# Kernel optimization log

Hardware: AMD Instinct MI355X
Metric: run time of the kernel (lower is better)

Reference implementation:

```python
import jax, jax.numpy as jnp
import numpy as np

B, T, C, HS = 4, 2048, 1024, 64

def setup_inputs() -> dict:
    key = jax.random.key(0)
    k1, k2, k3, k4 = jax.random.split(key, 4)
    x = jax.random.normal(k1, (B, T, C), dtype=jnp.float32)
    # torch Linear default init scale ~ 1/sqrt(fan_in); scale weights similarly
    s = C ** -0.5
    Wq = jax.random.normal(k2, (C, HS), dtype=jnp.float32) * s
    Wk = jax.random.normal(k3, (C, HS), dtype=jnp.float32) * s
    Wv = jax.random.normal(k4, (C, HS), dtype=jnp.float32) * s
    return {"x": x, "Wq": Wq, "Wk": Wk, "Wv": Wv}

def reference(x, Wq, Wk, Wv):
    B_, T_, C_ = x.shape
    q = x @ Wq          # [B,T,HS]
    k = x @ Wk          # [B,T,HS]
    v = x @ Wv          # [B,T,HS]
    scale = C_ ** -0.5  # note: module scales by input dim C, not head_size
    w = jnp.einsum('bqh,bkh->bqk', q, k) * scale  # [B,T,T]
    causal = jnp.tril(jnp.ones((T_, T_), dtype=bool))
    w = jnp.where(causal, w, -jnp.inf)
    a = jax.nn.softmax(w, axis=-1)  # dropout is identity (eval / drop_rate=0)
    return jnp.einsum('bqk,bkh->bqh', a, v)
```

## Files before the change

### kernel.cpp

```cpp
#include <hip/hip_runtime.h>
#include <math.h>

#define B_  4
#define T_  2048
#define C_  1024
#define HS_ 64
#define M_  (B_*T_)
#define NCAT 192
#define SCALE_ 0.03125f

typedef unsigned short ushort_t;
typedef short bf16x8 __attribute__((ext_vector_type(8)));
typedef float f32x4 __attribute__((ext_vector_type(4)));

static __device__ __forceinline__ unsigned short f2bf(float f) {
    union { float f; unsigned int u; } c; c.f = f;
    unsigned int u = c.u;
    return (unsigned short)((u + 0x7FFFu + ((u >> 16) & 1u)) >> 16);
}
static __device__ __forceinline__ unsigned short f2bf_fast(float f) {
    union { float f; unsigned int u; } c; c.f = f;
    return (unsigned short)((c.u + 0x8000u) >> 16);
}

__global__ void wconv_kernel(const float* __restrict__ Wq, const float* __restrict__ Wk,
                             const float* __restrict__ Wv, ushort_t* __restrict__ wt) {
    int idx = (blockIdx.x * 256 + threadIdx.x) * 4;
    int n = idx >> 10;
    int k0 = idx & 1023;
    const float* W = (n < 64) ? Wq : (n < 128) ? Wk : Wv;
    int nn = n & 63;
    ushort_t o0 = f2bf(W[(k0 + 0) * HS_ + nn]);
    ushort_t o1 = f2bf(W[(k0 + 1) * HS_ + nn]);
    ushort_t o2 = f2bf(W[(k0 + 2) * HS_ + nn]);
    ushort_t o3 = f2bf(W[(k0 + 3) * HS_ + nn]);
    uint2 d;
    d.x = (unsigned)o0 | ((unsigned)o1 << 16);
    d.y = (unsigned)o2 | ((unsigned)o3 << 16);
    *(uint2*)(wt + (size_t)n * C_ + k0) = d;
}

__global__ __launch_bounds__(512, 4) void proj_kernel(const float* __restrict__ x,
    const ushort_t* __restrict__ wt,
    ushort_t* __restrict__ qws, ushort_t* __restrict__ kws, ushort_t* __restrict__ vt) {
    __shared__ __align__(16) f32x4 red[4][12 * 64];

    int tid  = threadIdx.x;
    int wid  = tid >> 6;
    int lane = tid & 63;
    int qd   = lane >> 4;
    int lq   = lane & 15;
    int r0   = blockIdx.x * 16;

    f32x4 acc[12];
    #pragma unroll
    for (int i = 0; i < 12; i++) acc[i] = (f32x4){0.f,0.f,0.f,0.f};

    const float*    xp = x  + (size_t)(r0 + lq) * C_ + wid * 128 + qd * 8;
    const ushort_t* wp = wt + (size_t)lq * C_ + wid * 128 + qd * 8;

    #pragma unroll
    for (int i = 0; i < 4; i++) {
        float4 a0 = *(const float4*)(xp + i * 32);
        float4 a1 = *(const float4*)(xp + i * 32 + 4);
        union { bf16x8 v; ushort_t u[8]; } af;
        af.u[0] = f2bf(a0.x); af.u[1] = f2bf(a0.y); af.u[2] = f2bf(a0.z); af.u[3] = f2bf(a0.w);
        af.u[4] = f2bf(a1.x); af.u[5] = f2bf(a1.y); af.u[6] = f2bf(a1.z); af.u[7] = f2bf(a1.w);
        #pragma unroll
        for (int nt = 0; nt < 12; nt++) {
            bf16x8 bv = *(const bf16x8*)(wp + (size_t)nt * 16 * C_ + i * 32);
            acc[nt] = __builtin_amdgcn_mfma_f32_16x16x32_bf16(af.v, bv, acc[nt], 0, 0, 0);
        }
    }

    if (wid >= 4) {
        #pragma unroll
        for (int nt = 0; nt < 12; nt++) red[wid - 4][nt * 64 + lane] = acc[nt];
    }
    __syncthreads();
    if (wid < 4) {
        #pragma unroll
        for (int nt = 0; nt < 12; nt++) acc[nt] += red[wid][nt * 64 + lane];
    }
    __syncthreads();
    if (wid == 2 || wid == 3) {
        #pragma unroll
        for (int nt = 0; nt < 12; nt++) red[wid][nt * 64 + lane] = acc[nt];
    }
    __syncthreads();
    if (wid < 2) {
        #pragma unroll
        for (int nt = 0; nt < 12; nt++) acc[nt] += red[wid + 2][nt * 64 + lane];
    }
    __syncthreads();
    if (wid == 1) {
        #pragma unroll
        for (int nt = 0; nt < 12; nt++) red[0][nt * 64 + lane] = acc[nt];
    }
    __syncthreads();
    if (wid == 0) {
        #pragma unroll
        for (int nt = 0; nt < 12; nt++) {
            acc[nt] += red[0][nt * 64 + lane];
            int outn = nt >> 2;
            int col  = (nt & 3) * 16 + lq;
            #pragma unroll
            for (int r = 0; r < 4; r++) {
                int row = r0 + qd * 4 + r;
                float v = acc[nt][r];
                if (outn == 0) v *= SCALE_;
                ushort_t val = f2bf(v);
                if (outn == 0)      qws[(size_t)row * HS_ + col] = val;
                else if (outn == 1) kws[(size_t)row * HS_ + col] = val;
                else {
                    int b = row >> 11, t = row & 2047;
                    vt[((size_t)b * 64 + col) * T_ + t] = val;
                }
            }
        }
    }
}

__global__ __launch_bounds__(1024) void flash_kernel(const ushort_t* __restrict__ qws,
    const ushort_t* __restrict__ kws, const ushort_t* __restrict__ vt,
    float* __restrict__ out) {
    __shared__ __align__(16) unsigned char pool[36864];

    int tid  = threadIdx.x;
    int wid  = tid >> 6;
    int lane = tid & 63;
    int qd   = lane >> 4;
    int lq   = lane & 15;
    int ts   = wid >> 3;
    int ws   = wid & 7;

    int batch = blockIdx.y;
    int p     = blockIdx.x;
    int tile  = ts ? (127 - p) : p;
    int q0    = tile * 16;
    int qrow  = q0 + lq;
    int grow  = batch * T_ + qrow;
    int nU    = (q0 + 16 + 63) >> 6;

    bf16x8 qf[2];
    #pragma unroll
    for (int st = 0; st < 2; st++)
        qf[st] = *(const bf16x8*)(qws + (size_t)grow * HS_ + st * 32 + qd * 8);

    float lsum = 0.f;
    f32x4 O[4];
    #pragma unroll
    for (int nt = 0; nt < 4; nt++) O[nt] = (f32x4){0.f,0.f,0.f,0.f};

    ushort_t* pw = (ushort_t*)pool + wid * 1152 + lq * 72;
    const ushort_t* kp    = kws + (size_t)batch * T_ * HS_;
    const ushort_t* vbase = vt  + (size_t)batch * 64 * T_;

    for (int u = ws; u < nU; u += 8) {
        int kb = u * 64;

        bf16x8 kf[8];
        #pragma unroll
        for (int sub = 0; sub < 4; sub++)
            #pragma unroll
            for (int st = 0; st < 2; st++)
                kf[sub * 2 + st] = *(const bf16x8*)(kp + (size_t)(kb + sub * 16 + lq) * HS_ + st * 32 + qd * 8);

        f32x4 S[4];
        #pragma unroll
        for (int sub = 0; sub < 4; sub++) {
            f32x4 s = (f32x4){0.f,0.f,0.f,0.f};
            #pragma unroll
            for (int st = 0; st < 2; st++)
                s = __builtin_amdgcn_mfma_f32_16x16x32_bf16(kf[sub * 2 + st], qf[st], s, 0, 0, 0);
            S[sub] = s;
        }

        bf16x8 vf[8];
        #pragma unroll
        for (int nt = 0; nt < 4; nt++)
            #pragma unroll
            for (int kk = 0; kk < 2; kk++)
                vf[nt * 2 + kk] = *(const bf16x8*)(vbase + ((size_t)nt * 16 + lq) * T_ + kb + kk * 32 + qd * 8);

        if (kb + 64 > q0) {
            #pragma unroll
            for (int sub = 0; sub < 4; sub++)
                #pragma unroll
                for (int r = 0; r < 4; r++) {
                    int key = kb + sub * 16 + qd * 4 + r;
                    float pv = (key <= qrow) ? __expf(S[sub][r]) : 0.f;
                    S[sub][r] = pv;
                    lsum += pv;
                }
        } else {
            #pragma unroll
            for (int sub = 0; sub < 4; sub++)
                #pragma unroll
                for (int r = 0; r < 4; r++) {
                    float pv = __expf(S[sub][r]);
                    S[sub][r] = pv;
                    lsum += pv;
                }
        }

        #pragma unroll
        for (int sub = 0; sub < 4; sub++) {
            uint2 d;
            d.x = (unsigned)f2bf_fast(S[sub][0]) | ((unsigned)f2bf_fast(S[sub][1]) << 16);
            d.y = (unsigned)f2bf_fast(S[sub][2]) | ((unsigned)f2bf_fast(S[sub][3]) << 16);
            *(uint2*)(pw + sub * 16 + qd * 4) = d;
        }
        bf16x8 pf0 = *(const bf16x8*)(pw + qd * 8);
        bf16x8 pf1 = *(const bf16x8*)(pw + 32 + qd * 8);

        #pragma unroll
        for (int nt = 0; nt < 4; nt++) {
            O[nt] = __builtin_amdgcn_mfma_f32_16x16x32_bf16(vf[nt * 2 + 0], pf0, O[nt], 0, 0, 0);
            O[nt] = __builtin_amdgcn_mfma_f32_16x16x32_bf16(vf[nt * 2 + 1], pf1, O[nt], 0, 0, 0);
        }
    }

    f32x4* red  = (f32x4*)pool;
    float* lred = (float*)(pool + 32768);
    __syncthreads();
    if (ws >= 4) {
        int sl = ts * 4 + (ws - 4);
        f32x4* rs = red + (size_t)sl * 256;
        #pragma unroll
        for (int nt = 0; nt < 4; nt++) rs[nt * 64 + lane] = O[nt];
        lred[sl * 64 + lane] = lsum;
    }
    __syncthreads();
    if (ws < 4) {
        int sl = ts * 4 + ws;
        f32x4* rs = red + (size_t)sl * 256;
        #pragma unroll
        for (int nt = 0; nt < 4; nt++) O[nt] += rs[nt * 64 + lane];
        lsum += lred[sl * 64 + lane];
    }
    __syncthreads();
    if (ws == 2 || ws == 3) {
        int sl = ts * 4 + (ws - 2);
        f32x4* rs = red + (size_t)sl * 256;
        #pragma unroll
        for (int nt = 0; nt < 4; nt++) rs[nt * 64 + lane] = O[nt];
        lred[sl * 64 + lane] = lsum;
    }
    __syncthreads();
    if (ws < 2) {
        int sl = ts * 4 + ws;
        f32x4* rs = red + (size_t)sl * 256;
        #pragma unroll
        for (int nt = 0; nt < 4; nt++) O[nt] += rs[nt * 64 + lane];
        lsum += lred[sl * 64 + lane];
    }
    __syncthreads();
    if (ws == 1) {
        int sl = ts * 4;
        f32x4* rs = red + (size_t)sl * 256;
        #pragma unroll
        for (int nt = 0; nt < 4; nt++) rs[nt * 64 + lane] = O[nt];
        lred[sl * 64 + lane] = lsum;
    }
    __syncthreads();
    if (ws == 0) {
        int sl = ts * 4;
        f32x4* rs = red + (size_t)sl * 256;
        #pragma unroll
        for (int nt = 0; nt < 4; nt++) O[nt] += rs[nt * 64 + lane];
        lsum += lred[sl * 64 + lane];
        lsum += __shfl_xor(lsum, 16, 64);
        lsum += __shfl_xor(lsum, 32, 64);
        float li = 1.f / lsum;
        #pragma unroll
        for (int nt = 0; nt < 4; nt++) {
            f32x4 o = O[nt] * li;
            *(f32x4*)(out + (size_t)grow * HS_ + nt * 16 + qd * 4) = o;
        }
    }
}

extern "C" void kernel_launch(void* const* d_in, const int* in_sizes, int n_in,
                              void* d_out, int out_size, void* d_ws, size_t ws_size,
                              hipStream_t stream) {
    const float* x  = (const float*)d_in[0];
    const float* Wq = (const float*)d_in[1];
    const float* Wk = (const float*)d_in[2];
    const float* Wv = (const float*)d_in[3];
    float* out = (float*)d_out;

    ushort_t* wt  = (ushort_t*)d_ws;
    ushort_t* qws = wt  + (size_t)NCAT * C_;
    ushort_t* kws = qws + (size_t)M_ * HS_;
    ushort_t* vt  = kws + (size_t)M_ * HS_;

    wconv_kernel<<<NCAT * C_ / (256 * 4), 256, 0, stream>>>(Wq, Wk, Wv, wt);
    proj_kernel<<<512, 512, 0, stream>>>(x, wt, qws, kws, vt);
    flash_kernel<<<dim3(64, 4), 1024, 0, stream>>>(qws, kws, vt, out);
}
```

Before: 122.2 us.

## Fuse projection and flash attention into one kernel with per-tile ready flags

Merges the QKV projection kernel and the flash-attention kernel into a single 512-block launch. Each block first projects 16 rows and publishes a release flag, then runs attention for one 16-row query tile, spinning until the K/V tiles it needs are flagged ready. Work is spread by pairing tiles from the two halves of the sequence across blocks, with 8 waves per block instead of 16. V fragment loads are also split into two halves with a scheduling barrier to cut register pressure. The cost being targeted is the kernel boundary and the tail idle time between projection and attention; the risk is spin-wait deadlock or stalls if dependent blocks are not yet resident, and fewer waves per attention tile.

After: 383.2 us. 3.14x slower.

```diff
diff --git a/kernel.cpp b/kernel.cpp
--- a/kernel.cpp
+++ b/kernel.cpp
@@ -24,7 +24,12 @@
 }
 
 __global__ void wconv_kernel(const float* __restrict__ Wq, const float* __restrict__ Wk,
-                             const float* __restrict__ Wv, ushort_t* __restrict__ wt) {
+                             const float* __restrict__ Wv, ushort_t* __restrict__ wt,
+                             int* __restrict__ flags) {
+    if (blockIdx.x == 0) {
+        flags[threadIdx.x] = 0;
+        flags[threadIdx.x + 256] = 0;
+    }
     int idx = (blockIdx.x * 256 + threadIdx.x) * 4;
     int n = idx >> 10;
     int k0 = idx & 1023;
@@ -40,107 +45,119 @@
     *(uint2*)(wt + (size_t)n * C_ + k0) = d;
 }
 
-__global__ __launch_bounds__(512, 4) void proj_kernel(const float* __restrict__ x,
+__global__ __launch_bounds__(512, 4) void fused_kernel(const float* __restrict__ x,
     const ushort_t* __restrict__ wt,
-    ushort_t* __restrict__ qws, ushort_t* __restrict__ kws, ushort_t* __restrict__ vt) {
-    __shared__ __align__(16) f32x4 red[4][12 * 64];
+    ushort_t* __restrict__ qws, ushort_t* __restrict__ kws, ushort_t* __restrict__ vt,
+    int* __restrict__ flags, float* __restrict__ out) {
+    __shared__ __align__(16) unsigned char pool[49152];
 
     int tid  = threadIdx.x;
     int wid  = tid >> 6;
     int lane = tid & 63;
     int qd   = lane >> 4;
     int lq   = lane & 15;
-    int r0   = blockIdx.x * 16;
-
-    f32x4 acc[12];
-    #pragma unroll
-    for (int i = 0; i < 12; i++) acc[i] = (f32x4){0.f,0.f,0.f,0.f};
-
-    const float*    xp = x  + (size_t)(r0 + lq) * C_ + wid * 128 + qd * 8;
-    const ushort_t* wp = wt + (size_t)lq * C_ + wid * 128 + qd * 8;
-
-    #pragma unroll
-    for (int i = 0; i < 4; i++) {
-        float4 a0 = *(const float4*)(xp + i * 32);
-        float4 a1 = *(const float4*)(xp + i * 32 + 4);
-        union { bf16x8 v; ushort_t u[8]; } af;
-        af.u[0] = f2bf(a0.x); af.u[1] = f2bf(a0.y); af.u[2] = f2bf(a0.z); af.u[3] = f2bf(a0.w);
-        af.u[4] = f2bf(a1.x); af.u[5] = f2bf(a1.y); af.u[6] = f2bf(a1.z); af.u[7] = f2bf(a1.w);
-        #pragma unroll
-        for (int nt = 0; nt < 12; nt++) {
-            bf16x8 bv = *(const bf16x8*)(wp + (size_t)nt * 16 * C_ + i * 32);
-            acc[nt] = __builtin_amdgcn_mfma_f32_16x16x32_bf16(af.v, bv, acc[nt], 0, 0, 0);
-        }
-    }
-
-    if (wid >= 4) {
-        #pragma unroll
-        for (int nt = 0; nt < 12; nt++) red[wid - 4][nt * 64 + lane] = acc[nt];
-    }
-    __syncthreads();
-    if (wid < 4) {
-        #pragma unroll
-        for (int nt = 0; nt < 12; nt++) acc[nt] += red[wid][nt * 64 + lane];
-    }
-    __syncthreads();
-    if (wid == 2 || wid == 3) {
-        #pragma unroll
-        for (int nt = 0; nt < 12; nt++) red[wid][nt * 64 + lane] = acc[nt];
-    }
-    __syncthreads();
-    if (wid < 2) {
-        #pragma unroll
-        for (int nt = 0; nt < 12; nt++) acc[nt] += red[wid + 2][nt * 64 + lane];
-    }
-    __syncthreads();
-    if (wid == 1) {
-        #pragma unroll
-        for (int nt = 0; nt < 12; nt++) red[0][nt * 64 + lane] = acc[nt];
-    }
-    __syncthreads();
-    if (wid == 0) {
-        #pragma unroll
-        for (int nt = 0; nt < 12; nt++) {
-            acc[nt] += red[0][nt * 64 + lane];
-            int outn = nt >> 2;
-            int col  = (nt & 3) * 16 + lq;
-            #pragma unroll
-            for (int r = 0; r < 4; r++) {
-                int row = r0 + qd * 4 + r;
-                float v = acc[nt][r];
-                if (outn == 0) v *= SCALE_;
-                ushort_t val = f2bf(v);
-                if (outn == 0)      qws[(size_t)row * HS_ + col] = val;
-                else if (outn == 1) kws[(size_t)row * HS_ + col] = val;
-                else {
-                    int b = row >> 11, t = row & 2047;
-                    vt[((size_t)b * 64 + col) * T_ + t] = val;
+
+    {
+        f32x4 (*red)[12 * 64] = (f32x4 (*)[12 * 64])pool;
+        int r0 = blockIdx.x * 16;
+
+        f32x4 acc[12];
+        #pragma unroll
+        for (int i = 0; i < 12; i++) acc[i] = (f32x4){0.f,0.f,0.f,0.f};
+
+        const float*    xp = x  + (size_t)(r0 + lq) * C_ + wid * 128 + qd * 8;
+        const ushort_t* wp = wt + (size_t)lq * C_ + wid * 128 + qd * 8;
+
+        #pragma unroll
+        for (int i = 0; i < 4; i++) {
+            float4 a0 = *(const float4*)(xp + i * 32);
+            float4 a1 = *(const float4*)(xp + i * 32 + 4);
+            union { bf16x8 v; ushort_t u[8]; } af;
+            af.u[0] = f2bf(a0.x); af.u[1] = f2bf(a0.y); af.u[2] = f2bf(a0.z); af.u[3] = f2bf(a0.w);
+            af.u[4] = f2bf(a1.x); af.u[5] = f2bf(a1.y); af.u[6] = f2bf(a1.z); af.u[7] = f2bf(a1.w);
+            #pragma unroll
+            for (int nt = 0; nt < 12; nt++) {
+                bf16x8 bv = *(const bf16x8*)(wp + (size_t)nt * 16 * C_ + i * 32);
+                acc[nt] = __builtin_amdgcn_mfma_f32_16x16x32_bf16(af.v, bv, acc[nt], 0, 0, 0);
+            }
+        }
+
+        if (wid >= 4) {
+            #pragma unroll
+            for (int nt = 0; nt < 12; nt++) red[wid - 4][nt * 64 + lane] = acc[nt];
+        }
+        __syncthreads();
+        if (wid < 4) {
+            #pragma unroll
+            for (int nt = 0; nt < 12; nt++) acc[nt] += red[wid][nt * 64 + lane];
+        }
+        __syncthreads();
+        if (wid == 2 || wid == 3) {
+            #pragma unroll
+            for (int nt = 0; nt < 12; nt++) red[wid][nt * 64 + lane] = acc[nt];
+        }
+        __syncthreads();
+        if (wid < 2) {
+            #pragma unroll
+            for (int nt = 0; nt < 12; nt++) acc[nt] += red[wid + 2][nt * 64 + lane];
+        }
+        __syncthreads();
+        if (wid == 1) {
+            #pragma unroll
+            for (int nt = 0; nt < 12; nt++) red[0][nt * 64 + lane] = acc[nt];
+        }
+        __syncthreads();
+        if (wid == 0) {
+            #pragma unroll
+            for (int nt = 0; nt < 12; nt++) {
+                acc[nt] += red[0][nt * 64 + lane];
+                int outn = nt >> 2;
+                int col  = (nt & 3) * 16 + lq;
+                #pragma unroll
+                for (int r = 0; r < 4; r++) {
+                    int row = r0 + qd * 4 + r;
+                    float v = acc[nt][r];
+                    if (outn == 0) v *= SCALE_;
+                    ushort_t val = f2bf(v);
+                    if (outn == 0)      qws[(size_t)row * HS_ + col] = val;
+                    else if (outn == 1) kws[(size_t)row * HS_ + col] = val;
+                    else {
+                        int b = row >> 11, t = row & 2047;
+                        vt[((size_t)b * 64 + col) * T_ + t] = val;
+                    }
                 }
             }
-        }
-    }
-}
-
-__global__ __launch_bounds__(1024) void flash_kernel(const ushort_t* __restrict__ qws,
-    const ushort_t* __restrict__ kws, const ushort_t* __restrict__ vt,
-    float* __restrict__ out) {
-    __shared__ __align__(16) unsigned char pool[36864];
-
-    int tid  = threadIdx.x;
-    int wid  = tid >> 6;
-    int lane = tid & 63;
-    int qd   = lane >> 4;
-    int lq   = lane & 15;
-    int ts   = wid >> 3;
-    int ws   = wid & 7;
-
-    int batch = blockIdx.y;
-    int p     = blockIdx.x;
-    int tile  = ts ? (127 - p) : p;
+            __threadfence();
+            if (tid == 0)
+                __hip_atomic_store(&flags[blockIdx.x], 1, __ATOMIC_RELEASE,
+                                   __HIP_MEMORY_SCOPE_AGENT);
+        }
+    }
+
+    int bb    = (int)blockIdx.x;
+    int half  = bb >> 8;
+    int bl    = bb & 255;
+    int fbatch = bl >> 6;
+    int a     = bl & 63;
+    int tile  = half ? (63 - a) : (64 + a);
     int q0    = tile * 16;
     int qrow  = q0 + lq;
-    int grow  = batch * T_ + qrow;
-    int nU    = (q0 + 16 + 63) >> 6;
+    int grow  = fbatch * T_ + qrow;
+    int nU    = (tile + 4) >> 2;
+    int need  = nU * 4 - 1;
+    if (need > 127) need = 127;
+
+    if (tid == 0) {
+        const int* fb = flags + fbatch * 128;
+        int i = 0;
+        while (i <= need) {
+            if (__hip_atomic_load(&fb[i], __ATOMIC_ACQUIRE,
+                                  __HIP_MEMORY_SCOPE_AGENT) != 0) i++;
+        }
+    }
+    __syncthreads();
+
+    int ws = wid;
 
     bf16x8 qf[2];
     #pragma unroll
@@ -153,8 +170,8 @@
     for (int nt = 0; nt < 4; nt++) O[nt] = (f32x4){0.f,0.f,0.f,0.f};
 
     ushort_t* pw = (ushort_t*)pool + wid * 1152 + lq * 72;
-    const ushort_t* kp    = kws + (size_t)batch * T_ * HS_;
-    const ushort_t* vbase = vt  + (size_t)batch * 64 * T_;
+    const ushort_t* kp    = kws + (size_t)fbatch * T_ * HS_;
+    const ushort_t* vbase = vt  + (size_t)fbatch * 64 * T_;
 
     for (int u = ws; u < nU; u += 8) {
         int kb = u * 64;
@@ -175,13 +192,6 @@
                 s = __builtin_amdgcn_mfma_f32_16x16x32_bf16(kf[sub * 2 + st], qf[st], s, 0, 0, 0);
             S[sub] = s;
         }
-
-        bf16x8 vf[8];
-        #pragma unroll
-        for (int nt = 0; nt < 4; nt++)
-            #pragma unroll
-            for (int kk = 0; kk < 2; kk++)
-                vf[nt * 2 + kk] = *(const bf16x8*)(vbase + ((size_t)nt * 16 + lq) * T_ + kb + kk * 32 + qd * 8);
 
         if (kb + 64 > q0) {
             #pragma unroll
@@ -211,65 +221,70 @@
             d.y = (unsigned)f2bf_fast(S[sub][2]) | ((unsigned)f2bf_fast(S[sub][3]) << 16);
             *(uint2*)(pw + sub * 16 + qd * 4) = d;
         }
+        __builtin_amdgcn_sched_barrier(0);
+
         bf16x8 pf0 = *(const bf16x8*)(pw + qd * 8);
         bf16x8 pf1 = *(const bf16x8*)(pw + 32 + qd * 8);
 
         #pragma unroll
-        for (int nt = 0; nt < 4; nt++) {
-            O[nt] = __builtin_amdgcn_mfma_f32_16x16x32_bf16(vf[nt * 2 + 0], pf0, O[nt], 0, 0, 0);
-            O[nt] = __builtin_amdgcn_mfma_f32_16x16x32_bf16(vf[nt * 2 + 1], pf1, O[nt], 0, 0, 0);
+        for (int h = 0; h < 2; h++) {
+            bf16x8 vf[4];
+            #pragma unroll
+            for (int nt = 0; nt < 2; nt++)
+                #pragma unroll
+                for (int kk = 0; kk < 2; kk++)
+                    vf[nt * 2 + kk] = *(const bf16x8*)(vbase + ((size_t)(h * 2 + nt) * 16 + lq) * T_ + kb + kk * 32 + qd * 8);
+            #pragma unroll
+            for (int nt = 0; nt < 2; nt++) {
+                O[h * 2 + nt] = __builtin_amdgcn_mfma_f32_16x16x32_bf16(vf[nt * 2 + 0], pf0, O[h * 2 + nt], 0, 0, 0);
+                O[h * 2 + nt] = __builtin_amdgcn_mfma_f32_16x16x32_bf16(vf[nt * 2 + 1], pf1, O[h * 2 + nt], 0, 0, 0);
+            }
         }
     }
 
     f32x4* red  = (f32x4*)pool;
-    float* lred = (float*)(pool + 32768);
+    float* lred = (float*)(pool + 16384);
     __syncthreads();
     if (ws >= 4) {
-        int sl = ts * 4 + (ws - 4);
-        f32x4* rs = red + (size_t)sl * 256;
+        f32x4* rs = red + (size_t)(ws - 4) * 256;
         #pragma unroll
         for (int nt = 0; nt < 4; nt++) rs[nt * 64 + lane] = O[nt];
-        lred[sl * 64 + lane] = lsum;
+        lred[(ws - 4) * 64 + lane] = lsum;
     }
     __syncthreads();
     if (ws < 4) {
-        int sl = ts * 4 + ws;
-        f32x4* rs = red + (size_t)sl * 256;
+        f32x4* rs = red + (size_t)ws * 256;
         #pragma unroll
         for (int nt = 0; nt < 4; nt++) O[nt] += rs[nt * 64 + lane];
-        lsum += lred[sl * 64 + lane];
+        lsum += lred[ws * 64 + lane];
     }
     __syncthreads();
     if (ws == 2 || ws == 3) {
-        int sl = ts * 4 + (ws - 2);
-        f32x4* rs = red + (size_t)sl * 256;
+        f32x4* rs = red + (size_t)(ws - 2) * 256;
         #pragma unroll
         for (int nt = 0; nt < 4; nt++) rs[nt * 64 + lane] = O[nt];
-        lred[sl * 64 + lane] = lsum;
+        lred[(ws - 2) * 64 + lane] = lsum;
     }
     __syncthreads();
     if (ws < 2) {
-        int sl = ts * 4 + ws;
-        f32x4* rs = red + (size_t)sl * 256;
+        f32x4* rs = red + (size_t)ws * 256;
         #pragma unroll
         for (int nt = 0; nt < 4; nt++) O[nt] += rs[nt * 64 + lane];
-        lsum += lred[sl * 64 + lane];
+        lsum += lred[ws * 64 + lane];
     }
     __syncthreads();
     if (ws == 1) {
-        int sl = ts * 4;
-        f32x4* rs = red + (size_t)sl * 256;
+        f32x4* rs = red;
         #pragma unroll
         for (int nt = 0; nt < 4; nt++) rs[nt * 64 + lane] = O[nt];
-        lred[sl * 64 + lane] = lsum;
+        lred[lane] = lsum;
     }
     __syncthreads();
     if (ws == 0) {
-        int sl = ts * 4;
-        f32x4* rs = red + (size_t)sl * 256;
+        f32x4* rs = red;
         #pragma unroll
         for (int nt = 0; nt < 4; nt++) O[nt] += rs[nt * 64 + lane];
-        lsum += lred[sl * 64 + lane];
+        lsum += lred[lane];
         lsum += __shfl_xor(lsum, 16, 64);
         lsum += __shfl_xor(lsum, 32, 64);
         float li = 1.f / lsum;
@@ -294,8 +309,8 @@
     ushort_t* qws = wt  + (size_t)NCAT * C_;
     ushort_t* kws = qws + (size_t)M_ * HS_;
     ushort_t* vt  = kws + (size_t)M_ * HS_;
-
-    wconv_kernel<<<NCAT * C_ / (256 * 4), 256, 0, stream>>>(Wq, Wk, Wv, wt);
-    proj_kernel<<<512, 512, 0, stream>>>(x, wt, qws, kws, vt);
-    flash_kernel<<<dim3(64, 4), 1024, 0, stream>>>(qws, kws, vt, out);
-}
+    int* flags    = (int*)(vt + (size_t)M_ * HS_);
+
+    wconv_kernel<<<NCAT * C_ / (256 * 4), 256, 0, stream>>>(Wq, Wk, Wv, wt, flags);
+    fused_kernel<<<512, 512, 0, stream>>>(x, wt, qws, kws, vt, flags, out);
+}
```
